# Kernel optimization log

Hardware: AMD Instinct MI355X
Metric: run time of the kernel (lower is better)

The kernel has to match this reference:

```python
import jax, jax.numpy as jnp
import numpy as np

NUM_NODES = 40000
NUM_EDGES = 400000
DIM = 128
NUM_REL = 502  # num_relation * 2
NUM_HEAD = 1


def setup_inputs() -> dict:
    key = jax.random.key(0)
    ks = jax.random.split(key, 16)
    d = DIM
    return {
        "curr_stat": jax.random.normal(ks[0], (NUM_NODES, d), jnp.float32),
        "last_stat": jax.random.normal(ks[1], (NUM_NODES, d), jnp.float32),
        "relemb_weight": jax.random.normal(ks[2], (NUM_REL, d), jnp.float32),
        "selfrel_weight": jax.random.normal(ks[3], (1, d), jnp.float32),
        "Wq": jax.random.normal(ks[4], (2 * d, d), jnp.float32) * (1.0 / np.sqrt(2 * d)),
        "bq": jax.random.normal(ks[5], (d,), jnp.float32) * 0.02,
        "Wk": jax.random.normal(ks[6], (2 * d, d), jnp.float32) * (1.0 / np.sqrt(2 * d)),
        "bk": jax.random.normal(ks[7], (d,), jnp.float32) * 0.02,
        "Wv": jax.random.normal(ks[8], (d, d), jnp.float32) * (1.0 / np.sqrt(d)),
        "bv": jax.random.normal(ks[9], (d,), jnp.float32) * 0.02,
        "dyn_weight": jax.random.normal(ks[10], (d, d), jnp.float32) * (1.0 / np.sqrt(d)),
        "edge_index": jax.random.randint(ks[11], (2, NUM_EDGES), 0, NUM_NODES, jnp.int32),
        "edge_type": jax.random.randint(ks[12], (NUM_EDGES,), 0, NUM_REL, jnp.int32),
    }


def _segment_softmax(scores, seg, num_segments):
    # scores: [E, H]; softmax over edges sharing the same destination segment
    m = jax.ops.segment_max(scores, seg, num_segments=num_segments)  # [N, H]
    e = jnp.exp(scores - m[seg])
    s = jax.ops.segment_sum(e, seg, num_segments=num_segments)  # [N, H]
    return e / s[seg]


def reference(curr_stat, last_stat, relemb_weight, selfrel_weight,
              Wq, bq, Wk, bk, Wv, bv, dyn_weight,
              edge_index, edge_type):
    N, D = curr_stat.shape
    H = NUM_HEAD
    HD = D // H

    # append self-loop edges for every node, with the dedicated self-relation
    loop = jnp.arange(N, dtype=edge_index.dtype)
    src = jnp.concatenate([edge_index[0], loop])  # [E_total]
    dst = jnp.concatenate([edge_index[1], loop])  # [E_total]
    type_emb = jnp.concatenate(
        [relemb_weight[edge_type], jnp.broadcast_to(selfrel_weight, (N, D))], axis=0)

    E = src.shape[0]
    # linear projections (x @ W + b); torch Linear stores W transposed, same math
    q = (jnp.concatenate([curr_stat[dst], type_emb], -1) @ Wq + bq).reshape(E, H, HD)
    k = (jnp.concatenate([last_stat[src], type_emb], -1) @ Wk + bk).reshape(E, H, HD)
    v = (last_stat[src] @ Wv + bv).reshape(E, H, HD)

    attn = jnp.sum(q * k, axis=-1) / np.sqrt(HD).astype(np.float32)  # [E, H]

    dyn_prob = _segment_softmax(attn, dst, N)   # [E, H]
    sta_prob = _segment_softmax(-attn, dst, N)  # [E, H]

    counts = jax.ops.segment_sum(jnp.ones((E,), jnp.float32), dst, num_segments=N)
    denom = jnp.maximum(counts, 1.0)[:, None]  # scatter-mean denominator

    feat_dyn = jax.ops.segment_sum((dyn_prob[..., None] * v).reshape(E, D), dst,
                                   num_segments=N) / denom
    feat_sta = jax.ops.segment_sum((sta_prob[..., None] * v).reshape(E, D), dst,
                                   num_segments=N) / denom

    # stack (feat_sta, feat_dyn @ dyn_weight) -> [2, N, D]
    return jnp.stack([feat_sta, feat_dyn @ dyn_weight])
```

## Files before the change

### kernel.cpp

```cpp
#include <hip/hip_runtime.h>
#include <math.h>

#define DIMC 128

typedef __attribute__((ext_vector_type(8))) short short8;
typedef __attribute__((ext_vector_type(4))) float floatx4;

static __device__ __forceinline__ unsigned short f2bf(float x) {
    union { float f; unsigned int u; } v; v.f = x;
    unsigned int r = v.u + 0x7FFFu + ((v.u >> 16) & 1u);
    return (unsigned short)(r >> 16);
}
static __device__ __forceinline__ float2 bf2f2(unsigned int u) {
    union { unsigned int i; float f; } a, b;
    a.i = u << 16; b.i = u & 0xFFFF0000u;
    return make_float2(a.f, b.f);
}

struct PrepArgs { const float* W[4]; unsigned short* F[4]; };

__global__ __launch_bounds__(64) void prep_wfrag(PrepArgs a)
{
    int mat = blockIdx.y;
    int ts  = blockIdx.x;
    int s = ts & 3, t = ts >> 2;
    int lane = threadIdx.x;
    int q = lane >> 4, c = lane & 15;
    const float* W = a.W[mat];
    unsigned short o[8];
    #pragma unroll
    for (int j = 0; j < 8; ++j)
        o[j] = f2bf(W[(long)(s * 32 + q * 8 + j) * DIMC + t * 16 + c]);
    uint4 u;
    u.x = (unsigned)o[0] | ((unsigned)o[1] << 16);
    u.y = (unsigned)o[2] | ((unsigned)o[3] << 16);
    u.z = (unsigned)o[4] | ((unsigned)o[5] << 16);
    u.w = (unsigned)o[6] | ((unsigned)o[7] << 16);
    ((uint4*)a.F[mat])[ts * 64 + lane] = u;
}

struct GemmM3 {
    const float*          Af[3];
    const unsigned short* Ab[3];
    const unsigned short* F[3];
    const float*          bias[3];
    float*                outf[3];
    unsigned short*       outb[3];
};

__global__ __launch_bounds__(256) void gemm_mfma(GemmM3 g, int M)
{
    const int which = blockIdx.y;
    const float*          __restrict__ Af   = g.Af[which];
    const unsigned short* __restrict__ Ab   = g.Ab[which];
    const unsigned short* __restrict__ F    = g.F[which];
    const float*          __restrict__ bias = g.bias[which];
    float*          __restrict__ outf = g.outf[which];
    unsigned short* __restrict__ outb = g.outb[which];

    const int wave = threadIdx.x >> 6;
    const int lane = threadIdx.x & 63;
    const int q = lane >> 4, c = lane & 15;
    const int rowbase = blockIdx.x * 64 + wave * 16;

    short8 wf[8][4];
    const uint4* Fp = (const uint4*)F;
    #pragma unroll
    for (int t = 0; t < 8; ++t)
        #pragma unroll
        for (int s = 0; s < 4; ++s) {
            uint4 u = Fp[(t * 4 + s) * 64 + lane];
            wf[t][s] = *(short8*)&u;
        }

    floatx4 acc[8];
    #pragma unroll
    for (int t = 0; t < 8; ++t) {
        float b = bias ? bias[t * 16 + c] : 0.0f;
        acc[t] = (floatx4){b, b, b, b};
    }

    short8 af[4];
    if (Af) {
        const float* Ar = Af + (long)(rowbase + c) * DIMC + q * 8;
        #pragma unroll
        for (int s = 0; s < 4; ++s) {
            float4 x0 = *(const float4*)(Ar + s * 32);
            float4 x1 = *(const float4*)(Ar + s * 32 + 4);
            uint4 u;
            u.x = (unsigned)f2bf(x0.x) | ((unsigned)f2bf(x0.y) << 16);
            u.y = (unsigned)f2bf(x0.z) | ((unsigned)f2bf(x0.w) << 16);
            u.z = (unsigned)f2bf(x1.x) | ((unsigned)f2bf(x1.y) << 16);
            u.w = (unsigned)f2bf(x1.z) | ((unsigned)f2bf(x1.w) << 16);
            af[s] = *(short8*)&u;
        }
    } else {
        const unsigned short* Ar = Ab + (long)(rowbase + c) * DIMC + q * 8;
        #pragma unroll
        for (int s = 0; s < 4; ++s) {
            uint4 u = *(const uint4*)(Ar + s * 32);
            af[s] = *(short8*)&u;
        }
    }

    #pragma unroll
    for (int t = 0; t < 8; ++t)
        #pragma unroll
        for (int s = 0; s < 4; ++s)
            acc[t] = __builtin_amdgcn_mfma_f32_16x16x32_bf16(af[s], wf[t][s], acc[t], 0, 0, 0);

    if (outf) {
        #pragma unroll
        for (int t = 0; t < 8; ++t)
            #pragma unroll
            for (int r = 0; r < 4; ++r)
                outf[(long)(rowbase + q * 4 + r) * DIMC + t * 16 + c] = acc[t][r];
    } else {
        #pragma unroll
        for (int t = 0; t < 8; ++t)
            #pragma unroll
            for (int r = 0; r < 4; ++r) {
                unsigned int u = f2bf(acc[t][r]);
                unsigned int o = (unsigned int)__shfl_xor((int)u, 1);
                if ((lane & 1) == 0) {
                    unsigned int word = u | (o << 16);
                    ((unsigned int*)outb)[(long)(rowbase + q * 4 + r) * 64 + t * 8 + (c >> 1)] = word;
                }
            }
    }
}

__global__ __launch_bounds__(128) void rel_proj(
    const float* __restrict__ relemb, const float* __restrict__ selfrel,
    const float* __restrict__ Wq, const float* __restrict__ bq,
    const float* __restrict__ Wk, const float* __restrict__ bk,
    unsigned short* __restrict__ Qre, unsigned short* __restrict__ Kre, int R)
{
    int t = blockIdx.x;
    int c = threadIdx.x;
    const float* row = (t < R) ? (relemb + (long)t * DIMC) : selfrel;
    float aq = bq[c], ak = bk[c];
    for (int k = 0; k < DIMC; ++k) {
        float a = row[k];
        aq = fmaf(a, Wq[(long)(DIMC + k) * DIMC + c], aq);
        ak = fmaf(a, Wk[(long)(DIMC + k) * DIMC + c], ak);
    }
    Qre[(long)t * DIMC + c] = f2bf(aq);
    Kre[(long)t * DIMC + c] = f2bf(ak);
}

__global__ void zero_int(int* __restrict__ p, int n) {
    int i = blockIdx.x * blockDim.x + threadIdx.x;
    if (i < n) p[i] = 0;
}

__global__ void hist_kernel(const int* __restrict__ dst, int* __restrict__ deg, int E) {
    int e = blockIdx.x * blockDim.x + threadIdx.x;
    if (e < E) atomicAdd(&deg[dst[e]], 1);
}

__global__ __launch_bounds__(256) void partial_sums(const int* __restrict__ deg,
                                                    int* __restrict__ partial, int N)
{
    __shared__ int sh[256];
    int t = threadIdx.x;
    int beg = blockIdx.x * 1024 + t * 4;
    int s = 0;
    if (beg + 3 < N) { int4 v = *(const int4*)(deg + beg); s = v.x + v.y + v.z + v.w; }
    else { for (int j = 0; j < 4; ++j) if (beg + j < N) s += deg[beg + j]; }
    sh[t] = s;
    __syncthreads();
    for (int d = 128; d >= 1; d >>= 1) {
        if (t < d) sh[t] += sh[t + d];
        __syncthreads();
    }
    if (t == 0) partial[blockIdx.x] = sh[0];
}

__global__ __launch_bounds__(256) void scan_partials(int* __restrict__ partial, int nb)
{
    __shared__ int sh[256];
    int t = threadIdx.x;
    sh[t] = (t < nb) ? partial[t] : 0;
    __syncthreads();
    for (int d = 1; d < 256; d <<= 1) {
        int v = (t >= d) ? sh[t - d] : 0;
        __syncthreads();
        sh[t] += v;
        __syncthreads();
    }
    if (t < nb) partial[t] = (t == 0) ? 0 : sh[t - 1];
}

__global__ __launch_bounds__(256) void write_offsets(const int* __restrict__ deg,
                                                     const int* __restrict__ partial,
                                                     int* __restrict__ offs,
                                                     int* __restrict__ cursor, int N)
{
    __shared__ int sh[256];
    int t = threadIdx.x;
    int beg = blockIdx.x * 1024 + t * 4;
    int d0 = 0, d1 = 0, d2 = 0, d3 = 0;
    if (beg + 3 < N) { int4 v = *(const int4*)(deg + beg); d0 = v.x; d1 = v.y; d2 = v.z; d3 = v.w; }
    else {
        if (beg < N)     d0 = deg[beg];
        if (beg + 1 < N) d1 = deg[beg + 1];
        if (beg + 2 < N) d2 = deg[beg + 2];
        if (beg + 3 < N) d3 = deg[beg + 3];
    }
    int s = d0 + d1 + d2 + d3;
    sh[t] = s;
    __syncthreads();
    for (int d = 1; d < 256; d <<= 1) {
        int v = (t >= d) ? sh[t - d] : 0;
        __syncthreads();
        sh[t] += v;
        __syncthreads();
    }
    int base = partial[blockIdx.x] + sh[t] - s;
    int o0 = base, o1 = o0 + d0, o2 = o1 + d1, o3 = o2 + d2;
    if (beg < N)     { offs[beg]     = o0; cursor[beg]     = o0; }
    if (beg + 1 < N) { offs[beg + 1] = o1; cursor[beg + 1] = o1; }
    if (beg + 2 < N) { offs[beg + 2] = o2; cursor[beg + 2] = o2; }
    if (beg + 3 < N) { offs[beg + 3] = o3; cursor[beg + 3] = o3; }
}

__global__ void scatter_kernel(const int* __restrict__ src, const int* __restrict__ dst,
                               const int* __restrict__ etype, int* __restrict__ cursor,
                               int2* __restrict__ sedge, int E)
{
    int e = blockIdx.x * blockDim.x + threadIdx.x;
    if (e < E) {
        int d = dst[e];
        int p = atomicAdd(&cursor[d], 1);
        sedge[p] = make_int2(src[e], etype[e]);
    }
}

__global__ __launch_bounds__(256) void node_kernel(
    const float* __restrict__ Qn,
    const unsigned short* __restrict__ Kn, const unsigned short* __restrict__ Vn,
    const unsigned short* __restrict__ Qre, const unsigned short* __restrict__ Kre,
    const int* __restrict__ offs, const int* __restrict__ deg,
    const int2* __restrict__ sedge,
    float* __restrict__ out_sta, unsigned short* __restrict__ feat_dyn,
    int N, int R)
{
    int n = (blockIdx.x * blockDim.x + threadIdx.x) >> 6;
    int lane = threadIdx.x & 63;
    if (n >= N) return;

    const float scale = 0.08838834764831845f;
    int base = offs[n];
    int dcnt = deg[n];

    float2 qn = ((const float2*)(Qn + (long)n * DIMC))[lane];

    float2 ks = bf2f2(((const unsigned int*)(Kn + (long)n * DIMC))[lane]);
    float2 qr = bf2f2(((const unsigned int*)(Qre + (long)R * DIMC))[lane]);
    float2 kr = bf2f2(((const unsigned int*)(Kre + (long)R * DIMC))[lane]);
    float p = (qn.x + qr.x) * (ks.x + kr.x) + (qn.y + qr.y) * (ks.y + kr.y);
    #pragma unroll
    for (int m = 32; m >= 1; m >>= 1) p += __shfl_xor(p, m);
    float a_self = p * scale;

    float2 vs = bf2f2(((const unsigned int*)(Vn + (long)n * DIMC))[lane]);
    float m_dyn = a_self, s_dyn = 1.0f;
    float m_sta = -a_self, s_sta = 1.0f;
    float2 accd = vs;
    float2 accs = vs;

    int i = 0;
    for (; i + 4 <= dcnt; i += 4) {
        int2 e0 = sedge[base + i],     e1 = sedge[base + i + 1];
        int2 e2 = sedge[base + i + 2], e3 = sedge[base + i + 3];

        float2 kn0 = bf2f2(((const unsigned int*)(Kn + (long)e0.x * DIMC))[lane]);
        float2 kn1 = bf2f2(((const unsigned int*)(Kn + (long)e1.x * DIMC))[lane]);
        float2 kn2 = bf2f2(((const unsigned int*)(Kn + (long)e2.x * DIMC))[lane]);
        float2 kn3 = bf2f2(((const unsigned int*)(Kn + (long)e3.x * DIMC))[lane]);
        float2 q0 = bf2f2(((const unsigned int*)(Qre + (long)e0.y * DIMC))[lane]);
        float2 q1 = bf2f2(((const unsigned int*)(Qre + (long)e1.y * DIMC))[lane]);
        float2 q2 = bf2f2(((const unsigned int*)(Qre + (long)e2.y * DIMC))[lane]);
        float2 q3 = bf2f2(((const unsigned int*)(Qre + (long)e3.y * DIMC))[lane]);
        float2 k0 = bf2f2(((const unsigned int*)(Kre + (long)e0.y * DIMC))[lane]);
        float2 k1 = bf2f2(((const unsigned int*)(Kre + (long)e1.y * DIMC))[lane]);
        float2 k2 = bf2f2(((const unsigned int*)(Kre + (long)e2.y * DIMC))[lane]);
        float2 k3 = bf2f2(((const unsigned int*)(Kre + (long)e3.y * DIMC))[lane]);
        float2 v0 = bf2f2(((const unsigned int*)(Vn + (long)e0.x * DIMC))[lane]);
        float2 v1 = bf2f2(((const unsigned int*)(Vn + (long)e1.x * DIMC))[lane]);
        float2 v2 = bf2f2(((const unsigned int*)(Vn + (long)e2.x * DIMC))[lane]);
        float2 v3 = bf2f2(((const unsigned int*)(Vn + (long)e3.x * DIMC))[lane]);

        float p0 = (qn.x + q0.x) * (kn0.x + k0.x) + (qn.y + q0.y) * (kn0.y + k0.y);
        float p1 = (qn.x + q1.x) * (kn1.x + k1.x) + (qn.y + q1.y) * (kn1.y + k1.y);
        float p2 = (qn.x + q2.x) * (kn2.x + k2.x) + (qn.y + q2.y) * (kn2.y + k2.y);
        float p3 = (qn.x + q3.x) * (kn3.x + k3.x) + (qn.y + q3.y) * (kn3.y + k3.y);
        #pragma unroll
        for (int m = 32; m >= 1; m >>= 1) {
            p0 += __shfl_xor(p0, m);
            p1 += __shfl_xor(p1, m);
            p2 += __shfl_xor(p2, m);
            p3 += __shfl_xor(p3, m);
        }
        float a0 = p0 * scale, a1 = p1 * scale, a2 = p2 * scale, a3 = p3 * scale;

        float mx = fmaxf(fmaxf(a0, a1), fmaxf(a2, a3));
        float mn = fmaxf(m_dyn, mx);
        float f  = __expf(m_dyn - mn);
        float w0 = __expf(a0 - mn), w1 = __expf(a1 - mn);
        float w2 = __expf(a2 - mn), w3 = __expf(a3 - mn);
        s_dyn = fmaf(s_dyn, f, (w0 + w1) + (w2 + w3));
        accd.x = fmaf(accd.x, f, fmaf(w0, v0.x, fmaf(w1, v1.x, fmaf(w2, v2.x, w3 * v3.x))));
        accd.y = fmaf(accd.y, f, fmaf(w0, v0.y, fmaf(w1, v1.y, fmaf(w2, v2.y, w3 * v3.y))));
        m_dyn = mn;

        float nmx = -fminf(fminf(a0, a1), fminf(a2, a3));
        float ms = fmaxf(m_sta, nmx);
        float fs = __expf(m_sta - ms);
        float u0 = __expf(-a0 - ms), u1 = __expf(-a1 - ms);
        float u2 = __expf(-a2 - ms), u3 = __expf(-a3 - ms);
        s_sta = fmaf(s_sta, fs, (u0 + u1) + (u2 + u3));
        accs.x = fmaf(accs.x, fs, fmaf(u0, v0.x, fmaf(u1, v1.x, fmaf(u2, v2.x, u3 * v3.x))));
        accs.y = fmaf(accs.y, fs, fmaf(u0, v0.y, fmaf(u1, v1.y, fmaf(u2, v2.y, u3 * v3.y))));
        m_sta = ms;
    }

    for (; i < dcnt; ++i) {
        int2 e = sedge[base + i];
        float2 kn = bf2f2(((const unsigned int*)(Kn + (long)e.x * DIMC))[lane]);
        float2 q2 = bf2f2(((const unsigned int*)(Qre + (long)e.y * DIMC))[lane]);
        float2 k2 = bf2f2(((const unsigned int*)(Kre + (long)e.y * DIMC))[lane]);
        float pp = (qn.x + q2.x) * (kn.x + k2.x) + (qn.y + q2.y) * (kn.y + k2.y);
        #pragma unroll
        for (int m = 32; m >= 1; m >>= 1) pp += __shfl_xor(pp, m);
        float a = pp * scale;

        float2 v = bf2f2(((const unsigned int*)(Vn + (long)e.x * DIMC))[lane]);

        float mn = fmaxf(m_dyn, a);
        float fd = __expf(m_dyn - mn);
        float wd = __expf(a - mn);
        s_dyn = fmaf(s_dyn, fd, wd);
        accd.x = fmaf(accd.x, fd, wd * v.x);
        accd.y = fmaf(accd.y, fd, wd * v.y);
        m_dyn = mn;

        float ms = fmaxf(m_sta, -a);
        float fs = __expf(m_sta - ms);
        float ws_ = __expf(-a - ms);
        s_sta = fmaf(s_sta, fs, ws_);
        accs.x = fmaf(accs.x, fs, ws_ * v.x);
        accs.y = fmaf(accs.y, fs, ws_ * v.y);
        m_sta = ms;
    }

    float denom = (float)(dcnt + 1);
    float id_ = 1.0f / (s_dyn * denom);
    float is_ = 1.0f / (s_sta * denom);
    ((float2*)(out_sta + (long)n * DIMC))[lane] = make_float2(accs.x * is_, accs.y * is_);
    unsigned int pd = (unsigned)f2bf(accd.x * id_) | ((unsigned)f2bf(accd.y * id_) << 16);
    ((unsigned int*)feat_dyn)[(long)n * 64 + lane] = pd;
}

extern "C" void kernel_launch(void* const* d_in, const int* in_sizes, int n_in,
                              void* d_out, int out_size, void* d_ws, size_t ws_size,
                              hipStream_t stream)
{
    const float* curr    = (const float*)d_in[0];
    const float* last    = (const float*)d_in[1];
    const float* relemb  = (const float*)d_in[2];
    const float* selfrel = (const float*)d_in[3];
    const float* Wq      = (const float*)d_in[4];
    const float* bq      = (const float*)d_in[5];
    const float* Wk      = (const float*)d_in[6];
    const float* bk      = (const float*)d_in[7];
    const float* Wv      = (const float*)d_in[8];
    const float* bv      = (const float*)d_in[9];
    const float* dynw    = (const float*)d_in[10];
    const int*   eidx    = (const int*)d_in[11];
    const int*   etype   = (const int*)d_in[12];
    float* out = (float*)d_out;

    const int N = in_sizes[0] / DIMC;
    const int E = in_sizes[12];
    const int R = in_sizes[2] / DIMC;
    const int* esrc = eidx;
    const int* edst = eidx + E;

    char* wp = (char*)d_ws;
    auto alloc = [&](size_t bytes) { char* r = wp; wp += (bytes + 15) & ~(size_t)15; return r; };
    size_t nd = (size_t)N * DIMC;
    float*          Qn    = (float*)alloc(nd * 4);
    unsigned short* Knb   = (unsigned short*)alloc(nd * 2);
    unsigned short* Vnb   = (unsigned short*)alloc(nd * 2);
    unsigned short* Fdb   = (unsigned short*)alloc(nd * 2);
    unsigned short* Qreb  = (unsigned short*)alloc((size_t)(R + 1) * DIMC * 2);
    unsigned short* Kreb  = (unsigned short*)alloc((size_t)(R + 1) * DIMC * 2);
    unsigned short* FWq   = (unsigned short*)alloc(2048 * 8 * 2);
    unsigned short* FWk   = (unsigned short*)alloc(2048 * 8 * 2);
    unsigned short* FWv   = (unsigned short*)alloc(2048 * 8 * 2);
    unsigned short* FWd   = (unsigned short*)alloc(2048 * 8 * 2);
    int*            deg   = (int*)alloc((size_t)N * 4);
    int*            offs  = (int*)alloc((size_t)N * 4);
    int*            cursor= (int*)alloc((size_t)N * 4);
    int2*           sedge = (int2*)alloc((size_t)E * 8);
    int*            partial = (int*)alloc(256 * 4);

    const int gblk = N / 64;
    const int sblk = (N + 1023) / 1024;

    PrepArgs pa;
    pa.W[0] = Wq;   pa.F[0] = FWq;
    pa.W[1] = Wk;   pa.F[1] = FWk;
    pa.W[2] = Wv;   pa.F[2] = FWv;
    pa.W[3] = dynw; pa.F[3] = FWd;
    hipLaunchKernelGGL(prep_wfrag, dim3(32, 4), dim3(64), 0, stream, pa);

    GemmM3 qkv;
    qkv.Af[0] = curr; qkv.Ab[0] = nullptr; qkv.F[0] = FWq; qkv.bias[0] = nullptr; qkv.outf[0] = Qn;      qkv.outb[0] = nullptr;
    qkv.Af[1] = last; qkv.Ab[1] = nullptr; qkv.F[1] = FWk; qkv.bias[1] = nullptr; qkv.outf[1] = nullptr; qkv.outb[1] = Knb;
    qkv.Af[2] = last; qkv.Ab[2] = nullptr; qkv.F[2] = FWv; qkv.bias[2] = bv;      qkv.outf[2] = nullptr; qkv.outb[2] = Vnb;
    hipLaunchKernelGGL(gemm_mfma, dim3(gblk, 3), dim3(256), 0, stream, qkv, N);

    hipLaunchKernelGGL(rel_proj, dim3(R + 1), dim3(128), 0, stream,
                       relemb, selfrel, Wq, bq, Wk, bk, Qreb, Kreb, R);
    hipLaunchKernelGGL(zero_int, dim3((N + 255) / 256), dim3(256), 0, stream, deg, N);
    hipLaunchKernelGGL(hist_kernel, dim3((E + 255) / 256), dim3(256), 0, stream, edst, deg, E);
    hipLaunchKernelGGL(partial_sums, dim3(sblk), dim3(256), 0, stream, deg, partial, N);
    hipLaunchKernelGGL(scan_partials, dim3(1), dim3(256), 0, stream, partial, sblk);
    hipLaunchKernelGGL(write_offsets, dim3(sblk), dim3(256), 0, stream,
                       deg, partial, offs, cursor, N);
    hipLaunchKernelGGL(scatter_kernel, dim3((E + 255) / 256), dim3(256), 0, stream,
                       esrc, edst, etype, cursor, sedge, E);
    hipLaunchKernelGGL(node_kernel, dim3((N + 3) / 4), dim3(256), 0, stream,
                       Qn, Knb, Vnb, Qreb, Kreb, offs, deg, sedge, out, Fdb, N, R);

    GemmM3 fin;
    fin.Af[0] = nullptr; fin.Ab[0] = Fdb; fin.F[0] = FWd; fin.bias[0] = nullptr; fin.outf[0] = out + nd; fin.outb[0] = nullptr;
    fin.Af[1] = nullptr; fin.Ab[1] = Fdb; fin.F[1] = FWd; fin.bias[1] = nullptr; fin.outf[1] = out + nd; fin.outb[1] = nullptr;
    fin.Af[2] = nullptr; fin.Ab[2] = Fdb; fin.F[2] = FWd; fin.bias[2] = nullptr; fin.outf[2] = out + nd; fin.outb[2] = nullptr;
    hipLaunchKernelGGL(gemm_mfma, dim3(gblk, 1), dim3(256), 0, stream, fin, N);
}
```

Measured before the change: 248.6 us.

## Interleave K/V and Qre/Kre rows in bf16 and switch softmax to exp2

Node K and V projections are now stored interleaved in one buffer, and the relation Q and K projections likewise, so each gathered edge needs one 8-byte load per lane instead of two 4-byte loads to separate arrays. The attention scale folds in log2(e) so the softmax can use exp2f directly, and bf16 packing uses the hardware pair-conversion intrinsic. The GEMM gains a strided output mode to write the interleaved layout, which makes its bf16 stores non-contiguous.

```diff
diff --git a/kernel.cpp b/kernel.cpp
--- a/kernel.cpp
+++ b/kernel.cpp
@@ -1,4 +1,5 @@
 #include <hip/hip_runtime.h>
+#include <hip/hip_bf16.h>
 #include <math.h>
 
 #define DIMC 128
@@ -6,6 +7,10 @@
 typedef __attribute__((ext_vector_type(8))) short short8;
 typedef __attribute__((ext_vector_type(4))) float floatx4;
 
+static __device__ __forceinline__ unsigned pk2(float lo, float hi) {
+    __hip_bfloat162 h = __float22bfloat162_rn(make_float2(lo, hi));
+    return *(unsigned*)&h;
+}
 static __device__ __forceinline__ unsigned short f2bf(float x) {
     union { float f; unsigned int u; } v; v.f = x;
     unsigned int r = v.u + 0x7FFFu + ((v.u >> 16) & 1u);
@@ -46,6 +51,8 @@
     const float*          bias[3];
     float*                outf[3];
     unsigned short*       outb[3];
+    int                   ostride[3];
+    int                   ooff[3];
 };
 
 __global__ __launch_bounds__(256) void gemm_mfma(GemmM3 g, int M)
@@ -57,6 +64,8 @@
     const float*          __restrict__ bias = g.bias[which];
     float*          __restrict__ outf = g.outf[which];
     unsigned short* __restrict__ outb = g.outb[which];
+    const int ostride = g.ostride[which];
+    const int ooff    = g.ooff[which];
 
     const int wave = threadIdx.x >> 6;
     const int lane = threadIdx.x & 63;
@@ -88,10 +97,10 @@
             float4 x0 = *(const float4*)(Ar + s * 32);
             float4 x1 = *(const float4*)(Ar + s * 32 + 4);
             uint4 u;
-            u.x = (unsigned)f2bf(x0.x) | ((unsigned)f2bf(x0.y) << 16);
-            u.y = (unsigned)f2bf(x0.z) | ((unsigned)f2bf(x0.w) << 16);
-            u.z = (unsigned)f2bf(x1.x) | ((unsigned)f2bf(x1.y) << 16);
-            u.w = (unsigned)f2bf(x1.z) | ((unsigned)f2bf(x1.w) << 16);
+            u.x = pk2(x0.x, x0.y);
+            u.y = pk2(x0.z, x0.w);
+            u.z = pk2(x1.x, x1.y);
+            u.w = pk2(x1.z, x1.w);
             af[s] = *(short8*)&u;
         }
     } else {
@@ -120,11 +129,11 @@
         for (int t = 0; t < 8; ++t)
             #pragma unroll
             for (int r = 0; r < 4; ++r) {
-                unsigned int u = f2bf(acc[t][r]);
-                unsigned int o = (unsigned int)__shfl_xor((int)u, 1);
+                float other = __shfl_xor(acc[t][r], 1);
                 if ((lane & 1) == 0) {
-                    unsigned int word = u | (o << 16);
-                    ((unsigned int*)outb)[(long)(rowbase + q * 4 + r) * 64 + t * 8 + (c >> 1)] = word;
+                    unsigned word = pk2(acc[t][r], other);
+                    ((unsigned*)outb)[((long)(rowbase + q * 4 + r) * 64 + t * 8 + (c >> 1))
+                                      * (long)ostride + ooff] = word;
                 }
             }
     }
@@ -134,7 +143,7 @@
     const float* __restrict__ relemb, const float* __restrict__ selfrel,
     const float* __restrict__ Wq, const float* __restrict__ bq,
     const float* __restrict__ Wk, const float* __restrict__ bk,
-    unsigned short* __restrict__ Qre, unsigned short* __restrict__ Kre, int R)
+    uint2* __restrict__ QKre, int R)
 {
     int t = blockIdx.x;
     int c = threadIdx.x;
@@ -145,8 +154,10 @@
         aq = fmaf(a, Wq[(long)(DIMC + k) * DIMC + c], aq);
         ak = fmaf(a, Wk[(long)(DIMC + k) * DIMC + c], ak);
     }
-    Qre[(long)t * DIMC + c] = f2bf(aq);
-    Kre[(long)t * DIMC + c] = f2bf(ak);
+    float aqo = __shfl_xor(aq, 1);
+    float ako = __shfl_xor(ak, 1);
+    if ((c & 1) == 0)
+        QKre[(long)t * 64 + (c >> 1)] = make_uint2(pk2(aq, aqo), pk2(ak, ako));
 }
 
 __global__ void zero_int(int* __restrict__ p, int n) {
@@ -239,32 +250,32 @@
 
 __global__ __launch_bounds__(256) void node_kernel(
     const float* __restrict__ Qn,
-    const unsigned short* __restrict__ Kn, const unsigned short* __restrict__ Vn,
-    const unsigned short* __restrict__ Qre, const unsigned short* __restrict__ Kre,
+    const uint2* __restrict__ KV,
+    const uint2* __restrict__ QKre,
     const int* __restrict__ offs, const int* __restrict__ deg,
     const int2* __restrict__ sedge,
-    float* __restrict__ out_sta, unsigned short* __restrict__ feat_dyn,
+    float* __restrict__ out_sta, unsigned* __restrict__ feat_dyn,
     int N, int R)
 {
     int n = (blockIdx.x * blockDim.x + threadIdx.x) >> 6;
     int lane = threadIdx.x & 63;
     if (n >= N) return;
 
-    const float scale = 0.08838834764831845f;
+    const float cs = 0.08838834764831845f * 1.4426950408889634f;
     int base = offs[n];
     int dcnt = deg[n];
 
     float2 qn = ((const float2*)(Qn + (long)n * DIMC))[lane];
 
-    float2 ks = bf2f2(((const unsigned int*)(Kn + (long)n * DIMC))[lane]);
-    float2 qr = bf2f2(((const unsigned int*)(Qre + (long)R * DIMC))[lane]);
-    float2 kr = bf2f2(((const unsigned int*)(Kre + (long)R * DIMC))[lane]);
+    uint2 kvs = KV[(unsigned)n * 64u + lane];
+    uint2 qks = QKre[(unsigned)R * 64u + lane];
+    float2 ks = bf2f2(kvs.x), vs = bf2f2(kvs.y);
+    float2 qr = bf2f2(qks.x), kr = bf2f2(qks.y);
     float p = (qn.x + qr.x) * (ks.x + kr.x) + (qn.y + qr.y) * (ks.y + kr.y);
     #pragma unroll
     for (int m = 32; m >= 1; m >>= 1) p += __shfl_xor(p, m);
-    float a_self = p * scale;
-
-    float2 vs = bf2f2(((const unsigned int*)(Vn + (long)n * DIMC))[lane]);
+    float a_self = p * cs;
+
     float m_dyn = a_self, s_dyn = 1.0f;
     float m_sta = -a_self, s_sta = 1.0f;
     float2 accd = vs;
@@ -275,22 +286,23 @@
         int2 e0 = sedge[base + i],     e1 = sedge[base + i + 1];
         int2 e2 = sedge[base + i + 2], e3 = sedge[base + i + 3];
 
-        float2 kn0 = bf2f2(((const unsigned int*)(Kn + (long)e0.x * DIMC))[lane]);
-        float2 kn1 = bf2f2(((const unsigned int*)(Kn + (long)e1.x * DIMC))[lane]);
-        float2 kn2 = bf2f2(((const unsigned int*)(Kn + (long)e2.x * DIMC))[lane]);
-        float2 kn3 = bf2f2(((const unsigned int*)(Kn + (long)e3.x * DIMC))[lane]);
-        float2 q0 = bf2f2(((const unsigned int*)(Qre + (long)e0.y * DIMC))[lane]);
-        float2 q1 = bf2f2(((const unsigned int*)(Qre + (long)e1.y * DIMC))[lane]);
-        float2 q2 = bf2f2(((const unsigned int*)(Qre + (long)e2.y * DIMC))[lane]);
-        float2 q3 = bf2f2(((const unsigned int*)(Qre + (long)e3.y * DIMC))[lane]);
-        float2 k0 = bf2f2(((const unsigned int*)(Kre + (long)e0.y * DIMC))[lane]);
-        float2 k1 = bf2f2(((const unsigned int*)(Kre + (long)e1.y * DIMC))[lane]);
-        float2 k2 = bf2f2(((const unsigned int*)(Kre + (long)e2.y * DIMC))[lane]);
-        float2 k3 = bf2f2(((const unsigned int*)(Kre + (long)e3.y * DIMC))[lane]);
-        float2 v0 = bf2f2(((const unsigned int*)(Vn + (long)e0.x * DIMC))[lane]);
-        float2 v1 = bf2f2(((const unsigned int*)(Vn + (long)e1.x * DIMC))[lane]);
-        float2 v2 = bf2f2(((const unsigned int*)(Vn + (long)e2.x * DIMC))[lane]);
-        float2 v3 = bf2f2(((const unsigned int*)(Vn + (long)e3.x * DIMC))[lane]);
+        uint2 kv0 = KV[(unsigned)e0.x * 64u + lane];
+        uint2 kv1 = KV[(unsigned)e1.x * 64u + lane];
+        uint2 kv2 = KV[(unsigned)e2.x * 64u + lane];
+        uint2 kv3 = KV[(unsigned)e3.x * 64u + lane];
+        uint2 t0 = QKre[(unsigned)e0.y * 64u + lane];
+        uint2 t1 = QKre[(unsigned)e1.y * 64u + lane];
+        uint2 t2 = QKre[(unsigned)e2.y * 64u + lane];
+        uint2 t3 = QKre[(unsigned)e3.y * 64u + lane];
+
+        float2 kn0 = bf2f2(kv0.x), v0 = bf2f2(kv0.y);
+        float2 kn1 = bf2f2(kv1.x), v1 = bf2f2(kv1.y);
+        float2 kn2 = bf2f2(kv2.x), v2 = bf2f2(kv2.y);
+        float2 kn3 = bf2f2(kv3.x), v3 = bf2f2(kv3.y);
+        float2 q0 = bf2f2(t0.x), k0 = bf2f2(t0.y);
+        float2 q1 = bf2f2(t1.x), k1 = bf2f2(t1.y);
+        float2 q2 = bf2f2(t2.x), k2 = bf2f2(t2.y);
+        float2 q3 = bf2f2(t3.x), k3 = bf2f2(t3.y);
 
         float p0 = (qn.x + q0.x) * (kn0.x + k0.x) + (qn.y + q0.y) * (kn0.y + k0.y);
         float p1 = (qn.x + q1.x) * (kn1.x + k1.x) + (qn.y + q1.y) * (kn1.y + k1.y);
@@ -303,13 +315,13 @@
             p2 += __shfl_xor(p2, m);
             p3 += __shfl_xor(p3, m);
         }
-        float a0 = p0 * scale, a1 = p1 * scale, a2 = p2 * scale, a3 = p3 * scale;
+        float a0 = p0 * cs, a1 = p1 * cs, a2 = p2 * cs, a3 = p3 * cs;
 
         float mx = fmaxf(fmaxf(a0, a1), fmaxf(a2, a3));
         float mn = fmaxf(m_dyn, mx);
-        float f  = __expf(m_dyn - mn);
-        float w0 = __expf(a0 - mn), w1 = __expf(a1 - mn);
-        float w2 = __expf(a2 - mn), w3 = __expf(a3 - mn);
+        float f  = exp2f(m_dyn - mn);
+        float w0 = exp2f(a0 - mn), w1 = exp2f(a1 - mn);
+        float w2 = exp2f(a2 - mn), w3 = exp2f(a3 - mn);
         s_dyn = fmaf(s_dyn, f, (w0 + w1) + (w2 + w3));
         accd.x = fmaf(accd.x, f, fmaf(w0, v0.x, fmaf(w1, v1.x, fmaf(w2, v2.x, w3 * v3.x))));
         accd.y = fmaf(accd.y, f, fmaf(w0, v0.y, fmaf(w1, v1.y, fmaf(w2, v2.y, w3 * v3.y))));
@@ -317,9 +329,9 @@
 
         float nmx = -fminf(fminf(a0, a1), fminf(a2, a3));
         float ms = fmaxf(m_sta, nmx);
-        float fs = __expf(m_sta - ms);
-        float u0 = __expf(-a0 - ms), u1 = __expf(-a1 - ms);
-        float u2 = __expf(-a2 - ms), u3 = __expf(-a3 - ms);
+        float fs = exp2f(m_sta - ms);
+        float u0 = exp2f(-a0 - ms), u1 = exp2f(-a1 - ms);
+        float u2 = exp2f(-a2 - ms), u3 = exp2f(-a3 - ms);
         s_sta = fmaf(s_sta, fs, (u0 + u1) + (u2 + u3));
         accs.x = fmaf(accs.x, fs, fmaf(u0, v0.x, fmaf(u1, v1.x, fmaf(u2, v2.x, u3 * v3.x))));
         accs.y = fmaf(accs.y, fs, fmaf(u0, v0.y, fmaf(u1, v1.y, fmaf(u2, v2.y, u3 * v3.y))));
@@ -328,27 +340,26 @@
 
     for (; i < dcnt; ++i) {
         int2 e = sedge[base + i];
-        float2 kn = bf2f2(((const unsigned int*)(Kn + (long)e.x * DIMC))[lane]);
-        float2 q2 = bf2f2(((const unsigned int*)(Qre + (long)e.y * DIMC))[lane]);
-        float2 k2 = bf2f2(((const unsigned int*)(Kre + (long)e.y * DIMC))[lane]);
+        uint2 kv = KV[(unsigned)e.x * 64u + lane];
+        uint2 tt = QKre[(unsigned)e.y * 64u + lane];
+        float2 kn = bf2f2(kv.x), v = bf2f2(kv.y);
+        float2 q2 = bf2f2(tt.x), k2 = bf2f2(tt.y);
         float pp = (qn.x + q2.x) * (kn.x + k2.x) + (qn.y + q2.y) * (kn.y + k2.y);
         #pragma unroll
         for (int m = 32; m >= 1; m >>= 1) pp += __shfl_xor(pp, m);
-        float a = pp * scale;
-
-        float2 v = bf2f2(((const unsigned int*)(Vn + (long)e.x * DIMC))[lane]);
+        float a = pp * cs;
 
         float mn = fmaxf(m_dyn, a);
-        float fd = __expf(m_dyn - mn);
-        float wd = __expf(a - mn);
+        float fd = exp2f(m_dyn - mn);
+        float wd = exp2f(a - mn);
         s_dyn = fmaf(s_dyn, fd, wd);
         accd.x = fmaf(accd.x, fd, wd * v.x);
         accd.y = fmaf(accd.y, fd, wd * v.y);
         m_dyn = mn;
 
         float ms = fmaxf(m_sta, -a);
-        float fs = __expf(m_sta - ms);
-        float ws_ = __expf(-a - ms);
+        float fs = exp2f(m_sta - ms);
+        float ws_ = exp2f(-a - ms);
         s_sta = fmaf(s_sta, fs, ws_);
         accs.x = fmaf(accs.x, fs, ws_ * v.x);
         accs.y = fmaf(accs.y, fs, ws_ * v.y);
@@ -359,8 +370,7 @@
     float id_ = 1.0f / (s_dyn * denom);
     float is_ = 1.0f / (s_sta * denom);
     ((float2*)(out_sta + (long)n * DIMC))[lane] = make_float2(accs.x * is_, accs.y * is_);
-    unsigned int pd = (unsigned)f2bf(accd.x * id_) | ((unsigned)f2bf(accd.y * id_) << 16);
-    ((unsigned int*)feat_dyn)[(long)n * 64 + lane] = pd;
+    feat_dyn[(unsigned)n * 64u + lane] = pk2(accd.x * id_, accd.y * id_);
 }
 
 extern "C" void kernel_launch(void* const* d_in, const int* in_sizes, int n_in,
@@ -392,11 +402,9 @@
     auto alloc = [&](size_t bytes) { char* r = wp; wp += (bytes + 15) & ~(size_t)15; return r; };
     size_t nd = (size_t)N * DIMC;
     float*          Qn    = (float*)alloc(nd * 4);
-    unsigned short* Knb   = (unsigned short*)alloc(nd * 2);
-    unsigned short* Vnb   = (unsigned short*)alloc(nd * 2);
+    uint2*          KV    = (uint2*)alloc((size_t)N * 64 * 8);
     unsigned short* Fdb   = (unsigned short*)alloc(nd * 2);
-    unsigned short* Qreb  = (unsigned short*)alloc((size_t)(R + 1) * DIMC * 2);
-    unsigned short* Kreb  = (unsigned short*)alloc((size_t)(R + 1) * DIMC * 2);
+    uint2*          QKre  = (uint2*)alloc((size_t)(R + 1) * 64 * 8);
     unsigned short* FWq   = (unsigned short*)alloc(2048 * 8 * 2);
     unsigned short* FWk   = (unsigned short*)alloc(2048 * 8 * 2);
     unsigned short* FWv   = (unsigned short*)alloc(2048 * 8 * 2);
@@ -418,13 +426,16 @@
     hipLaunchKernelGGL(prep_wfrag, dim3(32, 4), dim3(64), 0, stream, pa);
 
     GemmM3 qkv;
-    qkv.Af[0] = curr; qkv.Ab[0] = nullptr; qkv.F[0] = FWq; qkv.bias[0] = nullptr; qkv.outf[0] = Qn;      qkv.outb[0] = nullptr;
-    qkv.Af[1] = last; qkv.Ab[1] = nullptr; qkv.F[1] = FWk; qkv.bias[1] = nullptr; qkv.outf[1] = nullptr; qkv.outb[1] = Knb;
-    qkv.Af[2] = last; qkv.Ab[2] = nullptr; qkv.F[2] = FWv; qkv.bias[2] = bv;      qkv.outf[2] = nullptr; qkv.outb[2] = Vnb;
+    qkv.Af[0] = curr; qkv.Ab[0] = nullptr; qkv.F[0] = FWq; qkv.bias[0] = nullptr;
+    qkv.outf[0] = Qn; qkv.outb[0] = nullptr; qkv.ostride[0] = 1; qkv.ooff[0] = 0;
+    qkv.Af[1] = last; qkv.Ab[1] = nullptr; qkv.F[1] = FWk; qkv.bias[1] = nullptr;
+    qkv.outf[1] = nullptr; qkv.outb[1] = (unsigned short*)KV; qkv.ostride[1] = 2; qkv.ooff[1] = 0;
+    qkv.Af[2] = last; qkv.Ab[2] = nullptr; qkv.F[2] = FWv; qkv.bias[2] = bv;
+    qkv.outf[2] = nullptr; qkv.outb[2] = (unsigned short*)KV; qkv.ostride[2] = 2; qkv.ooff[2] = 1;
     hipLaunchKernelGGL(gemm_mfma, dim3(gblk, 3), dim3(256), 0, stream, qkv, N);
 
     hipLaunchKernelGGL(rel_proj, dim3(R + 1), dim3(128), 0, stream,
-                       relemb, selfrel, Wq, bq, Wk, bk, Qreb, Kreb, R);
+                       relemb, selfrel, Wq, bq, Wk, bk, QKre, R);
     hipLaunchKernelGGL(zero_int, dim3((N + 255) / 256), dim3(256), 0, stream, deg, N);
     hipLaunchKernelGGL(hist_kernel, dim3((E + 255) / 256), dim3(256), 0, stream, edst, deg, E);
     hipLaunchKernelGGL(partial_sums, dim3(sblk), dim3(256), 0, stream, deg, partial, N);
@@ -434,11 +445,14 @@
     hipLaunchKernelGGL(scatter_kernel, dim3((E + 255) / 256), dim3(256), 0, stream,
                        esrc, edst, etype, cursor, sedge, E);
     hipLaunchKernelGGL(node_kernel, dim3((N + 3) / 4), dim3(256), 0, stream,
-                       Qn, Knb, Vnb, Qreb, Kreb, offs, deg, sedge, out, Fdb, N, R);
+                       Qn, KV, QKre, offs, deg, sedge, out, (unsigned*)Fdb, N, R);
 
     GemmM3 fin;
-    fin.Af[0] = nullptr; fin.Ab[0] = Fdb; fin.F[0] = FWd; fin.bias[0] = nullptr; fin.outf[0] = out + nd; fin.outb[0] = nullptr;
-    fin.Af[1] = nullptr; fin.Ab[1] = Fdb; fin.F[1] = FWd; fin.bias[1] = nullptr; fin.outf[1] = out + nd; fin.outb[1] = nullptr;
-    fin.Af[2] = nullptr; fin.Ab[2] = Fdb; fin.F[2] = FWd; fin.bias[2] = nullptr; fin.outf[2] = out + nd; fin.outb[2] = nullptr;
+    fin.Af[0] = nullptr; fin.Ab[0] = Fdb; fin.F[0] = FWd; fin.bias[0] = nullptr;
+    fin.outf[0] = out + nd; fin.outb[0] = nullptr; fin.ostride[0] = 1; fin.ooff[0] = 0;
+    fin.Af[1] = nullptr; fin.Ab[1] = Fdb; fin.F[1] = FWd; fin.bias[1] = nullptr;
+    fin.outf[1] = out + nd; fin.outb[1] = nullptr; fin.ostride[1] = 1; fin.ooff[1] = 0;
+    fin.Af[2] = nullptr; fin.Ab[2] = Fdb; fin.F[2] = FWd; fin.bias[2] = nullptr;
+    fin.outf[2] = out + nd; fin.outb[2] = nullptr; fin.ostride[2] = 1; fin.ooff[2] = 0;
     hipLaunchKernelGGL(gemm_mfma, dim3(gblk, 1), dim3(256), 0, stream, fin, N);
 }
```

After: 243.0 us. 2.2% less time.
